# Kernel optimization log

Hardware: AMD Instinct MI355X
Metric: run time of the kernel (lower is better)

The kernel has to match this reference:

```python
import jax, jax.numpy as jnp
import numpy as np
from jax import lax

EPS = 1e-5

def setup_inputs() -> dict:
    key = jax.random.key(0)
    k1, k2, k3 = jax.random.split(key, 3)
    B, S, D, W = 4, 4096, 2048, 4
    x = jax.random.normal(k1, (B, S, D), dtype=jnp.float32)
    norm_weight = jnp.ones((D,), dtype=jnp.float32)
    conv_weight = jax.random.normal(k2, (D, W), dtype=jnp.float32) * (1.0 / np.sqrt(W))
    proj_weight = jax.random.normal(k3, (2, D), dtype=jnp.float32) * (1.0 / np.sqrt(D))
    return {"x": x, "norm_weight": norm_weight, "conv_weight": conv_weight, "proj_weight": proj_weight}

def _rmsnorm(x, w):
    var = jnp.mean(x * x, axis=-1, keepdims=True)
    return x * lax.rsqrt(var + EPS) * w

def _causal_dw_conv_silu(h, conv_weight):
    # h: [B,S,D], conv_weight: [D,W]; causal depthwise conv along seq + silu
    B, S, D = h.shape
    W = conv_weight.shape[-1]
    hc = jnp.transpose(h, (0, 2, 1))                      # [B,D,S]
    hc = jnp.pad(hc, ((0, 0), (0, 0), (W - 1, 0)))        # left-pad for causality
    y = lax.conv_general_dilated(
        hc, conv_weight[:, None, :], window_strides=(1,), padding='VALID',
        dimension_numbers=('NCH', 'OIH', 'NCH'), feature_group_count=D)
    return jnp.transpose(jax.nn.silu(y), (0, 2, 1))       # [B,S,D]

def reference(x, norm_weight, conv_weight, proj_weight):
    B, S, D = x.shape
    h = _rmsnorm(x, norm_weight)
    h = _causal_dw_conv_silu(h, conv_weight)
    logits = jnp.einsum('bsd,od->bso', h, proj_weight)    # [B,S,2]
    gate = jax.nn.softmax(logits, axis=-1)[..., 1]        # [B,S]
    mask = gate > 0.5                                     # [B,S]
    # cumsum-index scatter-compress: selected tokens packed to the front,
    # unselected tokens routed to slot 0 which is dropped (padded to S, vs
    # data-dependent max_q in torch).
    idx = jnp.where(mask, jnp.cumsum(mask.astype(jnp.int32), axis=1), 0)  # [B,S]
    buf = jnp.zeros((B, S + 1, D), dtype=x.dtype)
    bidx = jnp.arange(B)[:, None]
    buf = buf.at[bidx, idx].set(x)
    return buf[:, 1:]
```

## Files before the change

### kernel.cpp

```cpp
#include <hip/hip_runtime.h>
#include <cstddef>

#define BATCH 4
#define SEQ   4096
#define DIM   2048
#define EPSF  1e-5f
#define TCHUNK 8
#define CPB   (SEQ / TCHUNK)
#define NBLK  (BATCH * CPB)

__device__ __forceinline__ float wave_sum(float v) {
#pragma unroll
    for (int off = 32; off > 0; off >>= 1)
        v += __shfl_down(v, off, 64);
    return v;
}
__device__ __forceinline__ int wave_sum_i(int v) {
#pragma unroll
    for (int off = 32; off > 0; off >>= 1)
        v += __shfl_down(v, off, 64);
    return v;
}

__global__ __launch_bounds__(256, 3) void mask_kernel(
    const float* __restrict__ x, const float* __restrict__ nw,
    const float* __restrict__ cw, const float* __restrict__ pw,
    unsigned int* __restrict__ cnt)
{
    __shared__ float lds_ss[3][4][4];
    __shared__ float lds_acc[2][4][4];

    const int t = threadIdx.x, lane = t & 63, wid = t >> 6;
    const int G = gridDim.x;
    const int chunk = (blockIdx.x & 7) * (G >> 3) + (blockIdx.x >> 3);
    const int b  = chunk / CPB;
    const int s0 = (chunk % CPB) * TCHUNK;
    const int d0 = 4 * t, d1 = d0 + 1024;

    float cwn[8][4], pd[8];
    {
        float4 n0 = *(const float4*)(nw + d0);
        float4 n1 = *(const float4*)(nw + d1);
        float nv[8] = {n0.x, n0.y, n0.z, n0.w, n1.x, n1.y, n1.z, n1.w};
#pragma unroll
        for (int i = 0; i < 8; ++i) {
            const int d = (i < 4) ? (d0 + i) : (d1 + i - 4);
            float4 c4 = *(const float4*)(cw + 4 * d);
            cwn[i][0] = c4.x * nv[i]; cwn[i][1] = c4.y * nv[i];
            cwn[i][2] = c4.z * nv[i]; cwn[i][3] = c4.w * nv[i];
        }
        float4 a0 = *(const float4*)(pw + d0);
        float4 a1 = *(const float4*)(pw + d1);
        float4 b0 = *(const float4*)(pw + DIM + d0);
        float4 b1 = *(const float4*)(pw + DIM + d1);
        pd[0] = b0.x - a0.x; pd[1] = b0.y - a0.y; pd[2] = b0.z - a0.z; pd[3] = b0.w - a0.w;
        pd[4] = b1.x - a1.x; pd[5] = b1.y - a1.y; pd[6] = b1.z - a1.z; pd[7] = b1.w - a1.w;
    }

    const float* xb = x + (size_t)b * SEQ * DIM;
    float h1[8], h2[8], h3[8];

    {
        float wv[3][8];
#pragma unroll
        for (int w = 0; w < 3; ++w) {
            const int s = s0 - 3 + w;
            if (s >= 0) {
                float4 a = *(const float4*)(xb + (size_t)s * DIM + d0);
                float4 c = *(const float4*)(xb + (size_t)s * DIM + d1);
                wv[w][0]=a.x; wv[w][1]=a.y; wv[w][2]=a.z; wv[w][3]=a.w;
                wv[w][4]=c.x; wv[w][5]=c.y; wv[w][6]=c.z; wv[w][7]=c.w;
            } else {
#pragma unroll
                for (int i = 0; i < 8; ++i) wv[w][i] = 0.f;
            }
            float ss = 0.f;
#pragma unroll
            for (int i = 0; i < 8; ++i) ss += wv[w][i] * wv[w][i];
            ss = wave_sum(ss);
            if (lane == 0) lds_ss[2][w][wid] = ss;
        }
        __syncthreads();
#pragma unroll
        for (int w = 0; w < 3; ++w) {
            const float sum4 = lds_ss[2][w][0] + lds_ss[2][w][1]
                             + lds_ss[2][w][2] + lds_ss[2][w][3];
            const float rstd = 1.0f / sqrtf(sum4 * (1.0f / DIM) + EPSF);
            float* h = (w == 0) ? h3 : (w == 1) ? h2 : h1;
#pragma unroll
            for (int i = 0; i < 8; ++i) h[i] = wv[w][i] * rstd;
        }
    }

#pragma unroll
    for (int g = 0; g < 2; ++g) {
        float xv[4][8];
#pragma unroll
        for (int j = 0; j < 4; ++j) {
            const int s = s0 + 4 * g + j;
            float4 a = *(const float4*)(xb + (size_t)s * DIM + d0);
            float4 c = *(const float4*)(xb + (size_t)s * DIM + d1);
            xv[j][0]=a.x; xv[j][1]=a.y; xv[j][2]=a.z; xv[j][3]=a.w;
            xv[j][4]=c.x; xv[j][5]=c.y; xv[j][6]=c.z; xv[j][7]=c.w;
        }
#pragma unroll
        for (int j = 0; j < 4; ++j) {
            float ss = 0.f;
#pragma unroll
            for (int i = 0; i < 8; ++i) ss += xv[j][i] * xv[j][i];
            ss = wave_sum(ss);
            if (lane == 0) lds_ss[g][j][wid] = ss;
        }
        __syncthreads();
#pragma unroll
        for (int j = 0; j < 4; ++j) {
            const float sum4 = lds_ss[g][j][0] + lds_ss[g][j][1]
                             + lds_ss[g][j][2] + lds_ss[g][j][3];
            const float rstd = 1.0f / sqrtf(sum4 * (1.0f / DIM) + EPSF);
            float acc = 0.f;
#pragma unroll
            for (int i = 0; i < 8; ++i) {
                const float hc = xv[j][i] * rstd;
                const float y = cwn[i][0] * h3[i] + cwn[i][1] * h2[i]
                              + cwn[i][2] * h1[i] + cwn[i][3] * hc;
                const float sig = 1.0f / (1.0f + __expf(-y));
                acc += (y * sig) * pd[i];
                h3[i] = h2[i]; h2[i] = h1[i]; h1[i] = hc;
            }
            acc = wave_sum(acc);
            if (lane == 0) lds_acc[g][j][wid] = acc;
        }
    }
    __syncthreads();

    if (wid == 0) {
        int sel = 0;
        if (lane < 8) {
            const int g = lane >> 2, j = lane & 3;
            const float a = lds_acc[g][j][0] + lds_acc[g][j][1]
                          + lds_acc[g][j][2] + lds_acc[g][j][3];
            sel = (a > 0.f) ? 1 : 0;
        }
        const unsigned long long bal = __ballot(sel);
        if (lane == 0)
            cnt[chunk] = (unsigned)__popcll(bal) | ((unsigned)(bal & 0xFFull) << 16);
    }
}

__global__ __launch_bounds__(256) void scatter_kernel(
    const float* __restrict__ x, const unsigned int* __restrict__ cnt,
    float* __restrict__ out)
{
    __shared__ unsigned int lds_r[4];
    const int blk  = blockIdx.x;
    const int b    = blk >> 9;
    const int cidx = blk & (CPB - 1);
    const int t = threadIdx.x, lane = t & 63, wid = t >> 6;

    const unsigned int* cb = cnt + b * CPB;
    const unsigned vown = cb[cidx];
    const unsigned bits = vown >> 16;

    const unsigned u0 = cb[t];
    const unsigned u1 = cb[256 + t];

    const int s0 = cidx * TCHUNK;
    const float* xb = x + (size_t)b * SEQ * DIM;
    const int d0 = 4 * t, d1 = d0 + 1024;
    const float4 z = make_float4(0.f, 0.f, 0.f, 0.f);
    float4 ra[TCHUNK], rc[TCHUNK];
#pragma unroll
    for (int j = 0; j < TCHUNK; ++j) {
        if ((bits >> j) & 1) {
            const float* src = xb + (size_t)(s0 + j) * DIM;
            ra[j] = *(const float4*)(src + d0);
            rc[j] = *(const float4*)(src + d1);
        } else { ra[j] = z; rc[j] = z; }
    }

    const int c0 = (int)(u0 & 0xFFFFu), c1 = (int)(u1 & 0xFFFFu);
    int pack = (((t < cidx) ? c0 : 0) + ((256 + t < cidx) ? c1 : 0))
             + ((c0 + c1) << 16);
    pack = wave_sum_i(pack);
    if (lane == 0) lds_r[wid] = (unsigned)pack;
    __syncthreads();
    const unsigned tot = lds_r[0] + lds_r[1] + lds_r[2] + lds_r[3];
    const int pre  = (int)(tot & 0xFFFFu);
    const int nsel = (int)(tot >> 16);

    float* ob = out + (size_t)b * SEQ * DIM;
#pragma unroll
    for (int j = 0; j < TCHUNK; ++j) {
        const int incl = __popc(bits & ((2u << j) - 1u));
        const int p    = pre + incl;
        const int sel  = (bits >> j) & 1;
        const int dest = sel ? (p - 1) : (nsel + s0 + j - p);
        float* o = ob + (size_t)dest * DIM;
        *(float4*)(o + d0) = ra[j];
        *(float4*)(o + d1) = rc[j];
    }
}

extern "C" void kernel_launch(void* const* d_in, const int* in_sizes, int n_in,
                              void* d_out, int out_size, void* d_ws, size_t ws_size,
                              hipStream_t stream) {
    const float* x  = (const float*)d_in[0];
    const float* nw = (const float*)d_in[1];
    const float* cw = (const float*)d_in[2];
    const float* pw = (const float*)d_in[3];
    float* out = (float*)d_out;

    unsigned int* cnt = (unsigned int*)d_ws;
    mask_kernel<<<NBLK, 256, 0, stream>>>(x, nw, cw, pw, cnt);
    scatter_kernel<<<NBLK, 256, 0, stream>>>(x, cnt, out);
}
```

Before: 263.4 us.

## Double mask-kernel chunk size, decouple scatter granularity, use nontemporal stores

```diff
diff --git a/kernel.cpp b/kernel.cpp
--- a/kernel.cpp
+++ b/kernel.cpp
@@ -5,9 +5,13 @@
 #define SEQ   4096
 #define DIM   2048
 #define EPSF  1e-5f
-#define TCHUNK 8
+#define TCHUNK 16
 #define CPB   (SEQ / TCHUNK)
 #define NBLK  (BATCH * CPB)
+#define SROWS 8
+#define NSCAT (BATCH * (SEQ / SROWS))
+
+typedef float f4 __attribute__((ext_vector_type(4)));
 
 __device__ __forceinline__ float wave_sum(float v) {
 #pragma unroll
@@ -22,13 +26,13 @@
     return v;
 }
 
-__global__ __launch_bounds__(256, 3) void mask_kernel(
+__global__ __launch_bounds__(256, 4) void mask_kernel(
     const float* __restrict__ x, const float* __restrict__ nw,
     const float* __restrict__ cw, const float* __restrict__ pw,
     unsigned int* __restrict__ cnt)
 {
-    __shared__ float lds_ss[3][4][4];
-    __shared__ float lds_acc[2][4][4];
+    __shared__ float lds_ss[5][4][4];
+    __shared__ float lds_acc[4][4][4];
 
     const int t = threadIdx.x, lane = t & 63, wid = t >> 6;
     const int G = gridDim.x;
@@ -78,13 +82,13 @@
 #pragma unroll
             for (int i = 0; i < 8; ++i) ss += wv[w][i] * wv[w][i];
             ss = wave_sum(ss);
-            if (lane == 0) lds_ss[2][w][wid] = ss;
+            if (lane == 0) lds_ss[4][w][wid] = ss;
         }
         __syncthreads();
 #pragma unroll
         for (int w = 0; w < 3; ++w) {
-            const float sum4 = lds_ss[2][w][0] + lds_ss[2][w][1]
-                             + lds_ss[2][w][2] + lds_ss[2][w][3];
+            const float sum4 = lds_ss[4][w][0] + lds_ss[4][w][1]
+                             + lds_ss[4][w][2] + lds_ss[4][w][3];
             const float rstd = 1.0f / sqrtf(sum4 * (1.0f / DIM) + EPSF);
             float* h = (w == 0) ? h3 : (w == 1) ? h2 : h1;
 #pragma unroll
@@ -93,7 +97,7 @@
     }
 
 #pragma unroll
-    for (int g = 0; g < 2; ++g) {
+    for (int g = 0; g < 4; ++g) {
         float xv[4][8];
 #pragma unroll
         for (int j = 0; j < 4; ++j) {
@@ -135,7 +139,7 @@
 
     if (wid == 0) {
         int sel = 0;
-        if (lane < 8) {
+        if (lane < 16) {
             const int g = lane >> 2, j = lane & 3;
             const float a = lds_acc[g][j][0] + lds_acc[g][j][1]
                           + lds_acc[g][j][2] + lds_acc[g][j][3];
@@ -143,34 +147,37 @@
         }
         const unsigned long long bal = __ballot(sel);
         if (lane == 0)
-            cnt[chunk] = (unsigned)__popcll(bal) | ((unsigned)(bal & 0xFFull) << 16);
-    }
-}
-
-__global__ __launch_bounds__(256) void scatter_kernel(
+            cnt[chunk] = (unsigned)__popcll(bal)
+                       | ((unsigned)(bal & 0xFFFFull) << 16);
+    }
+}
+
+__global__ __launch_bounds__(256, 4) void scatter_kernel(
     const float* __restrict__ x, const unsigned int* __restrict__ cnt,
     float* __restrict__ out)
 {
     __shared__ unsigned int lds_r[4];
     const int blk  = blockIdx.x;
     const int b    = blk >> 9;
-    const int cidx = blk & (CPB - 1);
+    const int c8   = blk & 511;
+    const int mc   = c8 >> 1;
+    const int hf   = c8 & 1;
     const int t = threadIdx.x, lane = t & 63, wid = t >> 6;
 
     const unsigned int* cb = cnt + b * CPB;
-    const unsigned vown = cb[cidx];
-    const unsigned bits = vown >> 16;
-
-    const unsigned u0 = cb[t];
-    const unsigned u1 = cb[256 + t];
-
-    const int s0 = cidx * TCHUNK;
+    const unsigned vown   = cb[mc];
+    const unsigned bits16 = vown >> 16;
+    const unsigned bits   = (bits16 >> (8 * hf)) & 0xFFu;
+
+    const unsigned u = cb[t];
+
+    const int s0 = c8 * SROWS;
     const float* xb = x + (size_t)b * SEQ * DIM;
     const int d0 = 4 * t, d1 = d0 + 1024;
     const float4 z = make_float4(0.f, 0.f, 0.f, 0.f);
-    float4 ra[TCHUNK], rc[TCHUNK];
-#pragma unroll
-    for (int j = 0; j < TCHUNK; ++j) {
+    float4 ra[SROWS], rc[SROWS];
+#pragma unroll
+    for (int j = 0; j < SROWS; ++j) {
         if ((bits >> j) & 1) {
             const float* src = xb + (size_t)(s0 + j) * DIM;
             ra[j] = *(const float4*)(src + d0);
@@ -178,26 +185,26 @@
         } else { ra[j] = z; rc[j] = z; }
     }
 
-    const int c0 = (int)(u0 & 0xFFFFu), c1 = (int)(u1 & 0xFFFFu);
-    int pack = (((t < cidx) ? c0 : 0) + ((256 + t < cidx) ? c1 : 0))
-             + ((c0 + c1) << 16);
+    const int c = (int)(u & 0xFFFFu);
+    int pack = ((t < mc) ? c : 0) + (c << 16);
     pack = wave_sum_i(pack);
     if (lane == 0) lds_r[wid] = (unsigned)pack;
     __syncthreads();
     const unsigned tot = lds_r[0] + lds_r[1] + lds_r[2] + lds_r[3];
-    const int pre  = (int)(tot & 0xFFFFu);
+    const int pre  = (int)(tot & 0xFFFFu)
+                   + (hf ? __popc(bits16 & 0xFFu) : 0);
     const int nsel = (int)(tot >> 16);
 
     float* ob = out + (size_t)b * SEQ * DIM;
 #pragma unroll
-    for (int j = 0; j < TCHUNK; ++j) {
+    for (int j = 0; j < SROWS; ++j) {
         const int incl = __popc(bits & ((2u << j) - 1u));
         const int p    = pre + incl;
         const int sel  = (bits >> j) & 1;
         const int dest = sel ? (p - 1) : (nsel + s0 + j - p);
         float* o = ob + (size_t)dest * DIM;
-        *(float4*)(o + d0) = ra[j];
-        *(float4*)(o + d1) = rc[j];
+        __builtin_nontemporal_store(*(const f4*)&ra[j], (f4*)(o + d0));
+        __builtin_nontemporal_store(*(const f4*)&rc[j], (f4*)(o + d1));
     }
 }
 
@@ -212,5 +219,5 @@
 
     unsigned int* cnt = (unsigned int*)d_ws;
     mask_kernel<<<NBLK, 256, 0, stream>>>(x, nw, cw, pw, cnt);
-    scatter_kernel<<<NBLK, 256, 0, stream>>>(x, cnt, out);
-}
+    scatter_kernel<<<NSCAT, 256, 0, stream>>>(x, cnt, out);
+}
```

Result: no change. 266.9 us (+1.3%).
